# Kernel optimization log

Measured on AMD Instinct MI355X. Metric: run time of the kernel, lower is better.

## Reference

```python
import jax, jax.numpy as jnp
import numpy as np

N = 100000
E = 1600000
H = 128


def setup_inputs() -> dict:
    key = jax.random.key(0)
    k1, k2, k3 = jax.random.split(key, 3)
    x = jax.random.normal(k1, (N, H), dtype=jnp.float32)
    edge_index = jax.random.randint(k2, (2, E), 0, N, dtype=jnp.int64)
    W = jax.random.normal(k3, (H, H), dtype=jnp.float32) / np.sqrt(H)
    b = jnp.zeros((H,), dtype=jnp.float32)
    gamma = jnp.ones((H,), dtype=jnp.float32)
    beta = jnp.zeros((H,), dtype=jnp.float32)
    return {"x": x, "edge_index": edge_index, "W": W, "b": b, "gamma": gamma, "beta": beta}


def reference(x, edge_index, W, b, gamma, beta):
    n = x.shape[0]
    # Linear transform first (standard GCNConv order)
    h = x @ W  # [N, H]
    # Add self loops
    loop = jnp.arange(n, dtype=edge_index.dtype)
    src = jnp.concatenate([edge_index[0], loop])
    dst = jnp.concatenate([edge_index[1], loop])
    # Symmetric degree normalization: deg computed over destination index
    ones = jnp.ones(src.shape[0], dtype=x.dtype)
    deg = jax.ops.segment_sum(ones, dst, num_segments=n)  # [N]
    dinv = jnp.where(deg > 0, jax.lax.rsqrt(deg), jnp.zeros_like(deg))
    norm = dinv[src] * dinv[dst]  # [E+N]
    # Gather, scale, scatter-add
    msgs = h[src] * norm[:, None]  # [E+N, H]
    out = jax.ops.segment_sum(msgs, dst, num_segments=n) + b  # [N, H]
    # GELU (exact erf form, matching torch F.gelu default)
    out = jax.nn.gelu(out, approximate=False)
    # LayerNorm over feature dim
    mu = jnp.mean(out, axis=-1, keepdims=True)
    var = jnp.mean(jnp.square(out - mu), axis=-1, keepdims=True)
    out = (out - mu) * jax.lax.rsqrt(var + 1e-5) * gamma + beta
    # Dropout is identity in eval mode
    return out
```

## Files before the change

kernel.cpp:

```cpp
#include <hip/hip_runtime.h>
#include <math.h>

#define H 128
#define PART_EDGES 4096
#define SORT_LDS 4096

typedef __bf16 bf16x8 __attribute__((ext_vector_type(8)));
typedef float f32x4 __attribute__((ext_vector_type(4)));
typedef _Float16 h2 __attribute__((ext_vector_type(2)));

static __device__ __forceinline__ unsigned short f2bf(float f) {
    unsigned u = __float_as_uint(f);
    unsigned r = 0x7fffu + ((u >> 16) & 1u);
    return (unsigned short)((u + r) >> 16);
}
static __device__ __forceinline__ unsigned packh2(float a, float b) {
    h2 h = { (_Float16)a, (_Float16)b };
    return __builtin_bit_cast(unsigned, h);
}
static __device__ __forceinline__ h2 u2h(unsigned w) {
    return __builtin_bit_cast(h2, w);
}

__global__ __launch_bounds__(256) void k_bhist(const int* __restrict__ dst,
                                               int* __restrict__ bcnt_pad,
                                               int E, int NBUK) {
    __shared__ int lh[1024];
    int t = threadIdx.x;
    for (int i = t; i < 1024; i += 256) lh[i] = 0;
    __syncthreads();
    int e0 = blockIdx.x * PART_EDGES;
    int e1 = min(e0 + PART_EDGES, E);
    for (int e = e0 + t; e < e1; e += 256) atomicAdd(&lh[dst[e] >> 7], 1);
    __syncthreads();
    for (int i = t; i < NBUK; i += 256) {
        int h = lh[i];
        if (h) atomicAdd(&bcnt_pad[i * 16], h);
    }
}

__global__ __launch_bounds__(1024) void k_bscan(const int* __restrict__ bcnt_pad,
                                                int* __restrict__ boff,
                                                int* __restrict__ bcur,
                                                int* __restrict__ rowp,
                                                int NBUK, int N, int E) {
    __shared__ int tmp[1024];
    __shared__ int carry;
    int t = threadIdx.x;
    if (t == 0) carry = 0;
    __syncthreads();
    for (int base = 0; base < NBUK; base += 1024) {
        int i = base + t;
        int v = (i < NBUK) ? bcnt_pad[i * 16] : 0;
        tmp[t] = v;
        __syncthreads();
#pragma unroll
        for (int off = 1; off < 1024; off <<= 1) {
            int a = (t >= off) ? tmp[t - off] : 0;
            __syncthreads();
            tmp[t] += a;
            __syncthreads();
        }
        int excl = carry + tmp[t] - v;
        if (i < NBUK) { boff[i] = excl; bcur[i] = excl; }
        __syncthreads();
        if (t == 1023) carry += tmp[1023];
        __syncthreads();
    }
    if (t == 0) { boff[NBUK] = carry; rowp[N] = E; }
}

__global__ void k_wt(const float* __restrict__ W, unsigned short* __restrict__ Wt) {
    int t = blockIdx.x * 256 + threadIdx.x;
    int j = t >> 7, k = t & 127;
    Wt[(size_t)j * H + k] = f2bf(W[(size_t)k * H + j]);
}

__global__ void k_xb(const float* __restrict__ x, const float* __restrict__ dinv,
                     unsigned* __restrict__ xb2, int N) {
    int t = blockIdx.x * 256 + threadIdx.x;
    if (t >= N * 32) return;
    int n = t >> 5;
    float s = dinv[n];
    float4 v = ((const float4*)x)[t];
    uint2 o;
    o.x = packh2(v.x * s, v.y * s);
    o.y = packh2(v.z * s, v.w * s);
    ((uint2*)xb2)[t] = o;
}

__global__ __launch_bounds__(256) void k_part(const int* __restrict__ ei,
                                              int* __restrict__ bcur,
                                              unsigned* __restrict__ pair, int E) {
    __shared__ int hist[1024];
    __shared__ int base[1024];
    int t = threadIdx.x;
    for (int i = t; i < 1024; i += 256) hist[i] = 0;
    __syncthreads();
    int e0 = blockIdx.x * PART_EDGES;
    int e1 = min(e0 + PART_EDGES, E);
    for (int e = e0 + t; e < e1; e += 256) {
        int d = ei[E + e];
        atomicAdd(&hist[d >> 7], 1);
    }
    __syncthreads();
    for (int i = t; i < 1024; i += 256) {
        int h = hist[i];
        base[i] = h ? atomicAdd(&bcur[i], h) : 0;
        hist[i] = 0;
    }
    __syncthreads();
    for (int e = e0 + t; e < e1; e += 256) {
        int s = ei[e];
        int d = ei[E + e];
        int b = d >> 7;
        int r = atomicAdd(&hist[b], 1);
        pair[base[b] + r] = (unsigned)s | ((unsigned)(d & 127) << 17);
    }
}

__global__ __launch_bounds__(256) void k_sort(const unsigned* __restrict__ pair,
                                              const int* __restrict__ boff,
                                              int* __restrict__ rowp,
                                              int* __restrict__ ssrc,
                                              float* __restrict__ dinv, int N) {
    __shared__ int hist[128];
    __shared__ int lofs[128];
    __shared__ int cur[128];
    __shared__ int sl[SORT_LDS];
    int b = blockIdx.x;
    int t = threadIdx.x;
    int lo = boff[b], hi = boff[b + 1];
    int cntE = hi - lo;
    if (t < 128) hist[t] = 0;
    __syncthreads();
    for (int i = t; i < cntE; i += 256) {
        unsigned w = pair[lo + i];
        atomicAdd(&hist[w >> 17], 1);
    }
    __syncthreads();
    int n0 = b << 7;
    if (t < 128 && n0 + t < N) dinv[n0 + t] = rsqrtf((float)(hist[t] + 1));
    if (t == 0) {
        int run = 0;
        for (int d = 0; d < 128; ++d) { lofs[d] = run; cur[d] = run; run += hist[d]; }
    }
    __syncthreads();
    if (t < 128 && n0 + t < N) rowp[n0 + t] = lo + lofs[t];
    for (int i = t; i < cntE; i += 256) {
        unsigned w = pair[lo + i];
        int d = w >> 17;
        int s = (int)(w & 0x1FFFF);
        int pos = atomicAdd(&cur[d], 1);
        if (pos < SORT_LDS) sl[pos] = s;
        else ssrc[lo + pos] = s;
    }
    __syncthreads();
    int lim = min(cntE, SORT_LDS);
    for (int i = t; i < lim; i += 256) ssrc[lo + i] = sl[i];
}

__global__ __launch_bounds__(256) void k_agg(const unsigned* __restrict__ xb2,
                                             const int* __restrict__ rowp,
                                             const int* __restrict__ ssrc,
                                             const float* __restrict__ dinv,
                                             unsigned* __restrict__ aggb2, int N) {
    int n = blockIdx.x * 4 + (threadIdx.x >> 6);
    if (n >= N) return;
    int lane = threadIdx.x & 63;
    int grp  = lane >> 4;
    int sub  = lane & 15;

    int lo = __builtin_amdgcn_readfirstlane(rowp[n]);
    int hi = __builtin_amdgcn_readfirstlane(rowp[n + 1]);
    float dn = dinv[n];

    h2 acc[4];
#pragma unroll
    for (int i = 0; i < 4; ++i) acc[i] = (h2){ (_Float16)0, (_Float16)0 };

    if (grp == 0) {
        uint4 sw = ((const uint4*)(xb2 + (size_t)n * 64))[sub];
        acc[0] = u2h(sw.x); acc[1] = u2h(sw.y);
        acc[2] = u2h(sw.z); acc[3] = u2h(sw.w);
    }

    for (int base = lo; base < hi; base += 64) {
        int take = hi - base; if (take > 64) take = 64;
        int sv = ssrc[base + (lane < take ? lane : take - 1)];

        int nFull = take >> 3;
        for (int it = 0; it < nFull; ++it) {
            int p1 = (it << 3) + grp;
            int p2 = p1 + 4;
            int s1 = __builtin_amdgcn_ds_bpermute(p1 << 2, sv);
            int s2 = __builtin_amdgcn_ds_bpermute(p2 << 2, sv);
            uint4 w1 = ((const uint4*)(xb2 + (size_t)s1 * 64))[sub];
            uint4 w2 = ((const uint4*)(xb2 + (size_t)s2 * 64))[sub];
            acc[0] += u2h(w1.x); acc[1] += u2h(w1.y);
            acc[2] += u2h(w1.z); acc[3] += u2h(w1.w);
            acc[0] += u2h(w2.x); acc[1] += u2h(w2.y);
            acc[2] += u2h(w2.z); acc[3] += u2h(w2.w);
        }
        if (take & 7) {
            int p1 = (nFull << 3) + grp;
            int p2 = p1 + 4;
            int q1 = (p1 < take) ? p1 : take - 1;
            int q2 = (p2 < take) ? p2 : take - 1;
            int s1 = __builtin_amdgcn_ds_bpermute(q1 << 2, sv);
            int s2 = __builtin_amdgcn_ds_bpermute(q2 << 2, sv);
            if (p1 < take) {
                uint4 w1 = ((const uint4*)(xb2 + (size_t)s1 * 64))[sub];
                acc[0] += u2h(w1.x); acc[1] += u2h(w1.y);
                acc[2] += u2h(w1.z); acc[3] += u2h(w1.w);
            }
            if (p2 < take) {
                uint4 w2 = ((const uint4*)(xb2 + (size_t)s2 * 64))[sub];
                acc[0] += u2h(w2.x); acc[1] += u2h(w2.y);
                acc[2] += u2h(w2.z); acc[3] += u2h(w2.w);
            }
        }
    }

#pragma unroll
    for (int i = 0; i < 4; ++i) {
        unsigned au = __builtin_bit_cast(unsigned, acc[i]);
        acc[i] += u2h((unsigned)__shfl_xor((int)au, 16, 64));
        au = __builtin_bit_cast(unsigned, acc[i]);
        acc[i] += u2h((unsigned)__shfl_xor((int)au, 32, 64));
    }

    if (grp == 0) {
        uint4 o;
        o.x = (unsigned)f2bf((float)acc[0][0] * dn) | ((unsigned)f2bf((float)acc[0][1] * dn) << 16);
        o.y = (unsigned)f2bf((float)acc[1][0] * dn) | ((unsigned)f2bf((float)acc[1][1] * dn) << 16);
        o.z = (unsigned)f2bf((float)acc[2][0] * dn) | ((unsigned)f2bf((float)acc[2][1] * dn) << 16);
        o.w = (unsigned)f2bf((float)acc[3][0] * dn) | ((unsigned)f2bf((float)acc[3][1] * dn) << 16);
        ((uint4*)(aggb2 + (size_t)n * 64))[sub] = o;
    }
}

__global__ __launch_bounds__(512) void k_gemm_ln(const unsigned short* __restrict__ aggb,
                                                 const unsigned short* __restrict__ Wt,
                                                 const float* __restrict__ bias,
                                                 const float* __restrict__ gamma,
                                                 const float* __restrict__ beta,
                                                 float* __restrict__ outp,
                                                 int N) {
    __shared__ unsigned short Ws[H * H];
    {
        const unsigned* src = (const unsigned*)Wt;
#pragma unroll
        for (int i = 0; i < 16; ++i) {
            int idx = threadIdx.x + i * 512;
            unsigned v = src[idx];
            int j = idx >> 6;
            int byte = (idx << 2) ^ ((j & 7) << 4);
            *(unsigned*)((char*)Ws + byte) = v;
        }
    }
    __syncthreads();

    const int wv   = threadIdx.x >> 6;
    const int lane = threadIdx.x & 63;
    const int g    = lane >> 4;
    const int c    = lane & 15;
    const int r0   = blockIdx.x * 128 + wv * 16;
    if (r0 >= N) return;

    float bc[8], gc[8], bec[8];
#pragma unroll
    for (int ct = 0; ct < 8; ++ct) {
        int col = ct * 16 + c;
        bc[ct]  = bias[col];
        gc[ct]  = gamma[col];
        bec[ct] = beta[col];
    }

    f32x4 acc[8];
#pragma unroll
    for (int ct = 0; ct < 8; ++ct) acc[ct] = (f32x4){0.f, 0.f, 0.f, 0.f};

#pragma unroll
    for (int ks = 0; ks < 4; ++ks) {
        int ar = r0 + c; if (ar >= N) ar = N - 1;
        bf16x8 af = *(const bf16x8*)(aggb + (size_t)ar * H + ks * 32 + g * 8);
#pragma unroll
        for (int ct = 0; ct < 8; ++ct) {
            int j = ct * 16 + c;
            int byte = (j * 256 + ks * 64 + g * 16) ^ ((j & 7) << 4);
            bf16x8 bf = *(const bf16x8*)((const char*)Ws + byte);
            acc[ct] = __builtin_amdgcn_mfma_f32_16x16x32_bf16(af, bf, acc[ct], 0, 0, 0);
        }
    }

#pragma unroll
    for (int q = 0; q < 4; ++q) {
        int row = r0 + g * 4 + q;
        float v[8];
        float s = 0.f, sq = 0.f;
#pragma unroll
        for (int ct = 0; ct < 8; ++ct) {
            float t = acc[ct][q] + bc[ct];
            t = 0.5f * t * (1.0f + erff(t * 0.70710678118654752f));
            v[ct] = t;
            s += t;
            sq += t * t;
        }
#pragma unroll
        for (int off = 8; off > 0; off >>= 1) {
            s  += __shfl_xor(s,  off, 64);
            sq += __shfl_xor(sq, off, 64);
        }
        float mu  = s * (1.0f / H);
        float var = sq * (1.0f / H) - mu * mu;
        float rs  = rsqrtf(var + 1e-5f);
        if (row < N) {
            float* op = outp + (size_t)row * H;
#pragma unroll
            for (int ct = 0; ct < 8; ++ct) {
                op[ct * 16 + c] = (v[ct] - mu) * rs * gc[ct] + bec[ct];
            }
        }
    }
}

extern "C" void kernel_launch(void* const* d_in, const int* in_sizes, int n_in,
                              void* d_out, int out_size, void* d_ws, size_t ws_size,
                              hipStream_t stream) {
    const float* x     = (const float*)d_in[0];
    const int*   ei    = (const int*)d_in[1];
    const float* W     = (const float*)d_in[2];
    const float* b     = (const float*)d_in[3];
    const float* gamma = (const float*)d_in[4];
    const float* beta  = (const float*)d_in[5];
    float* out = (float*)d_out;

    const int N = in_sizes[0] / H;
    const int E = in_sizes[1] / 2;
    const int NBUK = (N + 127) / 128;

    char* w = (char*)d_ws;
    auto alloc = [&](size_t bytes) {
        char* p = w;
        w += (bytes + 255) & ~(size_t)255;
        return p;
    };
    float* dinv     = (float*)alloc((size_t)N * 4);
    int*   bcnt_pad = (int*)alloc((size_t)NBUK * 16 * 4);
    int*   boff     = (int*)alloc((size_t)(NBUK + 1) * 4);
    int*   bcur     = (int*)alloc((size_t)NBUK * 4);
    int*   rowp     = (int*)alloc((size_t)(N + 1) * 4);
    int*   ssrc     = (int*)alloc((size_t)E * 4);
    unsigned short* Wt = (unsigned short*)alloc((size_t)H * H * 2);
    unsigned* aggb2 = (unsigned*)alloc((size_t)N * 64 * 4);

    unsigned* xb2  = (unsigned*)d_out;
    unsigned* pair = (unsigned*)d_out + (size_t)N * 64;

    k_wt   <<<(H * H) / 256, 256, 0, stream>>>(W, Wt);

    hipMemsetAsync(bcnt_pad, 0, (size_t)NBUK * 16 * 4, stream);
    k_bhist<<<(E + PART_EDGES - 1) / PART_EDGES, 256, 0, stream>>>(ei + E, bcnt_pad, E, NBUK);
    k_bscan<<<1, 1024, 0, stream>>>(bcnt_pad, boff, bcur, rowp, NBUK, N, E);
    k_part <<<(E + PART_EDGES - 1) / PART_EDGES, 256, 0, stream>>>(ei, bcur, pair, E);
    k_sort <<<NBUK, 256, 0, stream>>>(pair, boff, rowp, ssrc, dinv, N);
    k_xb   <<<(N * 32 + 255) / 256, 256, 0, stream>>>(x, dinv, xb2, N);

    k_agg  <<<(N + 3) / 4, 256, 0, stream>>>(xb2, rowp, ssrc, dinv, aggb2, N);

    k_gemm_ln<<<(N + 127) / 128, 512, 0, stream>>>((const unsigned short*)aggb2, Wt,
                                                   b, gamma, beta, out, N);
}
```

Baseline: 161.7 us.

## Pre-swizzle W, load it via direct global-to-LDS, fast GELU, larger partitions

Several independent changes. The transposed bf16 weight is written in already-swizzled order, so the GEMM kernel can copy it into LDS with global_load_lds (bypassing registers) while the activation fragments are prefetched up front. The library erff is replaced by an Abramowitz-Stegun polynomial with a fast exp, which cuts epilogue math but adds approximation error around 1e-7. The histogram and partition kernels process 8192 edges per block with 512 threads, halving block count and global bucket atomics.

```diff
diff --git a/kernel.cpp b/kernel.cpp
--- a/kernel.cpp
+++ b/kernel.cpp
@@ -2,12 +2,14 @@
 #include <math.h>
 
 #define H 128
-#define PART_EDGES 4096
+#define PART_EDGES 8192
 #define SORT_LDS 4096
 
 typedef __bf16 bf16x8 __attribute__((ext_vector_type(8)));
 typedef float f32x4 __attribute__((ext_vector_type(4)));
 typedef _Float16 h2 __attribute__((ext_vector_type(2)));
+typedef __attribute__((address_space(3))) unsigned lds_u32;
+typedef __attribute__((address_space(1))) const unsigned glob_u32;
 
 static __device__ __forceinline__ unsigned short f2bf(float f) {
     unsigned u = __float_as_uint(f);
@@ -21,19 +23,30 @@
 static __device__ __forceinline__ h2 u2h(unsigned w) {
     return __builtin_bit_cast(h2, w);
 }
-
-__global__ __launch_bounds__(256) void k_bhist(const int* __restrict__ dst,
+static __device__ __forceinline__ float gelu_f(float v) {
+    float z  = v * 0.70710678118654752f;
+    float az = fabsf(z);
+    float t  = __frcp_rn(1.0f + 0.3275911f * az);
+    float p  = t * (0.254829592f + t * (-0.284496736f + t * (1.421413741f +
+               t * (-1.453152027f + t * 1.061405429f))));
+    float e  = p * __expf(-az * az);
+    float erf = 1.0f - e;
+    erf = (z < 0.0f) ? -erf : erf;
+    return 0.5f * v * (1.0f + erf);
+}
+
+__global__ __launch_bounds__(512) void k_bhist(const int* __restrict__ dst,
                                                int* __restrict__ bcnt_pad,
                                                int E, int NBUK) {
     __shared__ int lh[1024];
     int t = threadIdx.x;
-    for (int i = t; i < 1024; i += 256) lh[i] = 0;
+    for (int i = t; i < 1024; i += 512) lh[i] = 0;
     __syncthreads();
     int e0 = blockIdx.x * PART_EDGES;
     int e1 = min(e0 + PART_EDGES, E);
-    for (int e = e0 + t; e < e1; e += 256) atomicAdd(&lh[dst[e] >> 7], 1);
-    __syncthreads();
-    for (int i = t; i < NBUK; i += 256) {
+    for (int e = e0 + t; e < e1; e += 512) atomicAdd(&lh[dst[e] >> 7], 1);
+    __syncthreads();
+    for (int i = t; i < NBUK; i += 512) {
         int h = lh[i];
         if (h) atomicAdd(&bcnt_pad[i * 16], h);
     }
@@ -70,10 +83,11 @@
     if (t == 0) { boff[NBUK] = carry; rowp[N] = E; }
 }
 
-__global__ void k_wt(const float* __restrict__ W, unsigned short* __restrict__ Wt) {
+__global__ void k_wt(const float* __restrict__ W, unsigned short* __restrict__ Wsz) {
     int t = blockIdx.x * 256 + threadIdx.x;
     int j = t >> 7, k = t & 127;
-    Wt[(size_t)j * H + k] = f2bf(W[(size_t)k * H + j]);
+    unsigned byte = (unsigned)(j * 256 + 2 * k) ^ (((unsigned)j & 7u) << 4);
+    *(unsigned short*)((char*)Wsz + byte) = f2bf(W[(size_t)k * H + j]);
 }
 
 __global__ void k_xb(const float* __restrict__ x, const float* __restrict__ dinv,
@@ -89,28 +103,28 @@
     ((uint2*)xb2)[t] = o;
 }
 
-__global__ __launch_bounds__(256) void k_part(const int* __restrict__ ei,
+__global__ __launch_bounds__(512) void k_part(const int* __restrict__ ei,
                                               int* __restrict__ bcur,
                                               unsigned* __restrict__ pair, int E) {
     __shared__ int hist[1024];
     __shared__ int base[1024];
     int t = threadIdx.x;
-    for (int i = t; i < 1024; i += 256) hist[i] = 0;
+    for (int i = t; i < 1024; i += 512) hist[i] = 0;
     __syncthreads();
     int e0 = blockIdx.x * PART_EDGES;
     int e1 = min(e0 + PART_EDGES, E);
-    for (int e = e0 + t; e < e1; e += 256) {
+    for (int e = e0 + t; e < e1; e += 512) {
         int d = ei[E + e];
         atomicAdd(&hist[d >> 7], 1);
     }
     __syncthreads();
-    for (int i = t; i < 1024; i += 256) {
+    for (int i = t; i < 1024; i += 512) {
         int h = hist[i];
         base[i] = h ? atomicAdd(&bcur[i], h) : 0;
         hist[i] = 0;
     }
     __syncthreads();
-    for (int e = e0 + t; e < e1; e += 256) {
+    for (int e = e0 + t; e < e1; e += 512) {
         int s = ei[e];
         int d = ei[E + e];
         int b = d >> 7;
@@ -241,85 +255,86 @@
 }
 
 __global__ __launch_bounds__(512) void k_gemm_ln(const unsigned short* __restrict__ aggb,
-                                                 const unsigned short* __restrict__ Wt,
+                                                 const unsigned short* __restrict__ Wsz,
                                                  const float* __restrict__ bias,
                                                  const float* __restrict__ gamma,
                                                  const float* __restrict__ beta,
                                                  float* __restrict__ outp,
                                                  int N) {
     __shared__ unsigned short Ws[H * H];
-    {
-        const unsigned* src = (const unsigned*)Wt;
-#pragma unroll
-        for (int i = 0; i < 16; ++i) {
-            int idx = threadIdx.x + i * 512;
-            unsigned v = src[idx];
-            int j = idx >> 6;
-            int byte = (idx << 2) ^ ((j & 7) << 4);
-            *(unsigned*)((char*)Ws + byte) = v;
-        }
-    }
-    __syncthreads();
 
     const int wv   = threadIdx.x >> 6;
     const int lane = threadIdx.x & 63;
     const int g    = lane >> 4;
     const int c    = lane & 15;
     const int r0   = blockIdx.x * 128 + wv * 16;
-    if (r0 >= N) return;
-
-    float bc[8], gc[8], bec[8];
-#pragma unroll
-    for (int ct = 0; ct < 8; ++ct) {
-        int col = ct * 16 + c;
-        bc[ct]  = bias[col];
-        gc[ct]  = gamma[col];
-        bec[ct] = beta[col];
-    }
-
-    f32x4 acc[8];
-#pragma unroll
-    for (int ct = 0; ct < 8; ++ct) acc[ct] = (f32x4){0.f, 0.f, 0.f, 0.f};
-
-#pragma unroll
-    for (int ks = 0; ks < 4; ++ks) {
-        int ar = r0 + c; if (ar >= N) ar = N - 1;
-        bf16x8 af = *(const bf16x8*)(aggb + (size_t)ar * H + ks * 32 + g * 8);
+
+    int ar = r0 + c; if (ar >= N) ar = N - 1;
+    bf16x8 af[4];
+#pragma unroll
+    for (int ks = 0; ks < 4; ++ks)
+        af[ks] = *(const bf16x8*)(aggb + (size_t)ar * H + ks * 32 + g * 8);
+
+#pragma unroll
+    for (int it = 0; it < 4; ++it) {
+        int off = it * 8192 + wv * 1024;
+        __builtin_amdgcn_global_load_lds(
+            (glob_u32*)((const char*)Wsz + off + lane * 16),
+            (lds_u32*)((char*)Ws + off), 16, 0, 0);
+    }
+    __syncthreads();
+
+    if (r0 < N) {
+        float bc[8], gc[8], bec[8];
 #pragma unroll
         for (int ct = 0; ct < 8; ++ct) {
-            int j = ct * 16 + c;
-            int byte = (j * 256 + ks * 64 + g * 16) ^ ((j & 7) << 4);
-            bf16x8 bf = *(const bf16x8*)((const char*)Ws + byte);
-            acc[ct] = __builtin_amdgcn_mfma_f32_16x16x32_bf16(af, bf, acc[ct], 0, 0, 0);
-        }
-    }
-
-#pragma unroll
-    for (int q = 0; q < 4; ++q) {
-        int row = r0 + g * 4 + q;
-        float v[8];
-        float s = 0.f, sq = 0.f;
-#pragma unroll
-        for (int ct = 0; ct < 8; ++ct) {
-            float t = acc[ct][q] + bc[ct];
-            t = 0.5f * t * (1.0f + erff(t * 0.70710678118654752f));
-            v[ct] = t;
-            s += t;
-            sq += t * t;
-        }
-#pragma unroll
-        for (int off = 8; off > 0; off >>= 1) {
-            s  += __shfl_xor(s,  off, 64);
-            sq += __shfl_xor(sq, off, 64);
-        }
-        float mu  = s * (1.0f / H);
-        float var = sq * (1.0f / H) - mu * mu;
-        float rs  = rsqrtf(var + 1e-5f);
-        if (row < N) {
-            float* op = outp + (size_t)row * H;
+            int col = ct * 16 + c;
+            bc[ct]  = bias[col];
+            gc[ct]  = gamma[col];
+            bec[ct] = beta[col];
+        }
+
+        f32x4 acc[8];
+#pragma unroll
+        for (int ct = 0; ct < 8; ++ct) acc[ct] = (f32x4){0.f, 0.f, 0.f, 0.f};
+
+#pragma unroll
+        for (int ks = 0; ks < 4; ++ks) {
 #pragma unroll
             for (int ct = 0; ct < 8; ++ct) {
-                op[ct * 16 + c] = (v[ct] - mu) * rs * gc[ct] + bec[ct];
+                int j = ct * 16 + c;
+                int byte = (j * 256 + ks * 64 + g * 16) ^ ((j & 7) << 4);
+                bf16x8 bf = *(const bf16x8*)((const char*)Ws + byte);
+                acc[ct] = __builtin_amdgcn_mfma_f32_16x16x32_bf16(af[ks], bf, acc[ct], 0, 0, 0);
+            }
+        }
+
+#pragma unroll
+        for (int q = 0; q < 4; ++q) {
+            int row = r0 + g * 4 + q;
+            float v[8];
+            float s = 0.f, sq = 0.f;
+#pragma unroll
+            for (int ct = 0; ct < 8; ++ct) {
+                float t = gelu_f(acc[ct][q] + bc[ct]);
+                v[ct] = t;
+                s += t;
+                sq += t * t;
+            }
+#pragma unroll
+            for (int off = 8; off > 0; off >>= 1) {
+                s  += __shfl_xor(s,  off, 64);
+                sq += __shfl_xor(sq, off, 64);
+            }
+            float mu  = s * (1.0f / H);
+            float var = sq * (1.0f / H) - mu * mu;
+            float rs  = rsqrtf(var + 1e-5f);
+            if (row < N) {
+                float* op = outp + (size_t)row * H;
+#pragma unroll
+                for (int ct = 0; ct < 8; ++ct) {
+                    op[ct * 16 + c] = (v[ct] - mu) * rs * gc[ct] + bec[ct];
+                }
             }
         }
     }
@@ -352,23 +367,23 @@
     int*   bcur     = (int*)alloc((size_t)NBUK * 4);
     int*   rowp     = (int*)alloc((size_t)(N + 1) * 4);
     int*   ssrc     = (int*)alloc((size_t)E * 4);
-    unsigned short* Wt = (unsigned short*)alloc((size_t)H * H * 2);
+    unsigned short* Wsz = (unsigned short*)alloc((size_t)H * H * 2);
     unsigned* aggb2 = (unsigned*)alloc((size_t)N * 64 * 4);
 
     unsigned* xb2  = (unsigned*)d_out;
     unsigned* pair = (unsigned*)d_out + (size_t)N * 64;
 
-    k_wt   <<<(H * H) / 256, 256, 0, stream>>>(W, Wt);
+    k_wt   <<<(H * H) / 256, 256, 0, stream>>>(W, Wsz);
 
     hipMemsetAsync(bcnt_pad, 0, (size_t)NBUK * 16 * 4, stream);
-    k_bhist<<<(E + PART_EDGES - 1) / PART_EDGES, 256, 0, stream>>>(ei + E, bcnt_pad, E, NBUK);
+    k_bhist<<<(E + PART_EDGES - 1) / PART_EDGES, 512, 0, stream>>>(ei + E, bcnt_pad, E, NBUK);
     k_bscan<<<1, 1024, 0, stream>>>(bcnt_pad, boff, bcur, rowp, NBUK, N, E);
-    k_part <<<(E + PART_EDGES - 1) / PART_EDGES, 256, 0, stream>>>(ei, bcur, pair, E);
+    k_part <<<(E + PART_EDGES - 1) / PART_EDGES, 512, 0, stream>>>(ei, bcur, pair, E);
     k_sort <<<NBUK, 256, 0, stream>>>(pair, boff, rowp, ssrc, dinv, N);
     k_xb   <<<(N * 32 + 255) / 256, 256, 0, stream>>>(x, dinv, xb2, N);
 
     k_agg  <<<(N + 3) / 4, 256, 0, stream>>>(xb2, rowp, ssrc, dinv, aggb2, N);
 
-    k_gemm_ln<<<(N + 127) / 128, 512, 0, stream>>>((const unsigned short*)aggb2, Wt,
+    k_gemm_ln<<<(N + 127) / 128, 512, 0, stream>>>((const unsigned short*)aggb2, Wsz,
                                                    b, gamma, beta, out, N);
 }
```

Measured after the change: 152.4 us. 5.7% less time.
